# Kernel optimization log

Hardware: AMD Instinct MI355X
Metric: run time of the kernel (lower is better)

The kernel has to match this reference:

```python
import jax, jax.numpy as jnp
import numpy as np

B, L = 64, 200
NQ = 1024          # n_question == output_dim
NPID = 4096
D = 256            # q_embed_dim
H = 512            # hidden_dim
Q = 1024           # output_dim
L2 = 1e-05


def setup_inputs() -> dict:
    key = jax.random.key(0)
    ks = jax.random.split(key, 20)
    q_data = jax.random.randint(ks[0], (B, L), 1, NQ + 1)          # question ids in [1, NQ]
    ans = jax.random.randint(ks[1], (B, L), 0, 2)
    qa_data = q_data + NQ * ans                                     # encoded (q, answer)
    pid_data = jax.random.randint(ks[2], (B, L), 0, NPID + 1)
    matrix = jax.random.uniform(ks[3], (Q, Q), jnp.float32) * 0.05  # p_c_relations
    u = jax.random.uniform(ks[4], (B, L))
    target = jnp.where(u < 0.1, -1.0, jnp.where(u < 0.55, 0.0, 1.0)).astype(jnp.float32)
    s = 0.05
    q_emb = jax.random.normal(ks[5], (NQ + 1, D), jnp.float32) * s
    qa_emb = jax.random.normal(ks[6], (2, D), jnp.float32) * s
    q_emb_diff = jax.random.normal(ks[7], (NQ + 1, D), jnp.float32) * s
    qa_emb_diff = jax.random.normal(ks[8], (2 * NQ + 1, D), jnp.float32) * s
    diff_parm = jax.random.normal(ks[9], (NPID + 1, 1), jnp.float32) * s
    gs = 1.0 / np.sqrt(H).astype(np.float32)
    w_ih = jax.random.uniform(ks[10], (3 * H, 2 * D), jnp.float32, -gs, gs)
    w_hh = jax.random.uniform(ks[11], (3 * H, H), jnp.float32, -gs, gs)
    b_ih = jax.random.uniform(ks[12], (3 * H,), jnp.float32, -gs, gs)
    b_hh = jax.random.uniform(ks[13], (3 * H,), jnp.float32, -gs, gs)
    fc_w = jax.random.normal(ks[14], (Q, H), jnp.float32) * 0.02
    fc_b = jnp.zeros((Q,), jnp.float32)
    return dict(q_data=q_data, qa_data=qa_data, pid_data=pid_data, matrix=matrix,
                target=target, q_emb=q_emb, qa_emb=qa_emb, q_emb_diff=q_emb_diff,
                qa_emb_diff=qa_emb_diff, diff_parm=diff_parm, w_ih=w_ih, w_hh=w_hh,
                b_ih=b_ih, b_hh=b_hh, fc_w=fc_w, fc_b=fc_b)


def _gru(x, w_ih, w_hh, b_ih, b_hh):
    # PyTorch GRU, single layer, batch_first. x: [B, L, In]
    xg = jnp.einsum('bli,gi->blg', x, w_ih) + b_ih          # [B, L, 3H]
    def step(h, xg_t):
        hg = h @ w_hh.T + b_hh
        xr, xz, xn = jnp.split(xg_t, 3, axis=-1)
        hr, hz, hn = jnp.split(hg, 3, axis=-1)
        r = jax.nn.sigmoid(xr + hr)
        z = jax.nn.sigmoid(xz + hz)
        n = jnp.tanh(xn + r * hn)
        h_new = (1.0 - z) * n + z * h
        return h_new, h_new
    h0 = jnp.zeros((x.shape[0], w_hh.shape[1]), x.dtype)
    _, hs = jax.lax.scan(step, h0, xg.transpose(1, 0, 2))
    return hs.transpose(1, 0, 2)                             # [B, L, H]


def reference(q_data, qa_data, pid_data, matrix, target, q_emb, qa_emb,
              q_emb_diff, qa_emb_diff, diff_parm, w_ih, w_hh, b_ih, b_hh,
              fc_w, fc_b):
    q_embed = q_emb[q_data]                                  # [B, L, D]
    qa = (qa_data - q_data) // NQ                            # answer in {0,1}
    qa_embed = qa_emb[qa] + q_embed
    pid_embed = diff_parm[pid_data]                          # [B, L, 1]
    q_embed2 = q_embed + pid_embed * q_emb_diff[q_data]
    qa_embed2 = qa_embed + pid_embed * qa_emb_diff[qa]
    c_reg = (pid_embed ** 2).sum() * L2

    x = jnp.concatenate([qa_embed2, q_embed2], axis=-1)      # [B, L, 2D]
    gru_out = _gru(x, w_ih, w_hh, b_ih, b_hh)
    gru_out = jnp.einsum('blh,qh->blq', gru_out, fc_w) + fc_b  # [B, L, Q]

    got = jnp.einsum('blq,kq->blk', gru_out, matrix)         # [B, L, Q]
    master = jnp.where(got >= 0.4, 1.0, got)                 # threshold-to-1 only
    # mastery of the question asked at step t: master[b, t, q-1]
    mvals = jnp.take_along_axis(master, (q_data - 1)[..., None], axis=2)[..., 0]  # [B, L]

    f32 = jnp.float32
    eq = (q_data[:, :, None] == q_data[:, None, :]).astype(f32)   # [B, t, k]
    t_idx = jnp.arange(L)
    tri_strict = (t_idx[:, None] > t_idx[None, :]).astype(f32)    # k < t
    tri_incl = (t_idx[:, None] >= t_idx[None, :]).astype(f32)     # k <= t
    mast = (mvals == 1.0).astype(f32)
    notm = (mvals == 0.0).astype(f32)
    qa1 = (qa == 1).astype(f32)
    qa0 = 1.0 - qa1
    base = eq * tri_strict                                        # [B, L, L]
    mc = jnp.einsum('btk,bk->bt', base, qa1 * mast)   # master_correct
    mi = jnp.einsum('btk,bk->bt', base, qa0 * mast)   # master_incorrect
    nmc = jnp.einsum('btk,bk->bt', base, qa0 * notm)  # no_master_correct
    aa = jnp.einsum('btk,tk->bt', eq, tri_incl)       # answered_all (>= 1)

    arB = jnp.arange(B)
    idx = q_data - 1

    def dina_step(carry, xs):
        guess, slip = carry                            # [B, Q] each
        i_t, m_t, qa_t, mc_t, mi_t, nmc_t, aa_t = xs   # [B] each
        g_upd = jnp.where(m_t == 1.0, mc_t / aa_t,
                          jnp.where(qa_t == 0, 1.0 - nmc_t / aa_t, nmc_t / aa_t))
        upd_slip = (m_t == 1.0) & (qa_t == 0)
        new_g = jnp.where(upd_slip, guess[arB, i_t], g_upd)
        new_s = jnp.where(upd_slip, mi_t / aa_t, slip[arB, i_t])
        guess = guess.at[arB, i_t].set(new_g)
        slip = slip.at[arB, i_t].set(new_s)
        p = (1.0 - new_s) * (m_t * new_g + (1.0 - new_s) * (1.0 - m_t))
        return (guess, slip), p

    init = (jnp.zeros((B, Q), f32), jnp.zeros((B, Q), f32))
    xs = (idx.T, mvals.T, qa.T, mc.T, mi.T, nmc.T, aa.T)
    _, ps = jax.lax.scan(dina_step, init, xs)          # [L, B]
    preds = ps.T.reshape(-1)                           # [B*L]

    labels = target.reshape(-1)
    mask = labels > -0.9
    preds_d = jax.lax.stop_gradient(preds)             # torch detaches via torch.tensor()
    mse_sum = (((preds_d - labels) ** 2) * mask.astype(f32)).sum()
    loss = mse_sum + c_reg
    return (loss, jax.nn.sigmoid(preds_d), mask.sum())
```

## Files before the change

### kernel.cpp

```cpp
#include <hip/hip_runtime.h>
#include <hip/hip_bf16.h>
#include <math.h>

#define BB 64
#define LL 200
#define NQ 1024
#define DD 256
#define HH 512
#define QQ 1024
#define G3 1536
#define BL 12800
#define GBLK 256

#define OFF_ACC   ((size_t)0)
#define OFF_CELLS ((size_t)16)
#define OFF_HA    ((size_t)1056)
#define OFF_AQ    (OFF_HA + 65536)
#define OFF_DQ    (OFF_AQ + 1574400)
#define OFF_BQA   (OFF_DQ + 1574400)
#define OFF_CQA   (OFF_BQA + 3072)
#define OFF_WSUM  (OFF_CQA + 3072)
#define OFF_FCWT  (OFF_WSUM + 393216)
#define OFF_M2    (OFF_FCWT + 524288)
#define OFF_MB    (OFF_M2 + 524288)
#define OFF_XG    (OFF_MB + 1024)
#define OFF_GRUT  (OFF_XG + 19660800)
#define OFF_QINT  (OFF_GRUT + 6553600)
#define OFF_QAINT (OFF_QINT + 12800)
#define OFF_PIDF  (OFF_QAINT + 12800)
#define OFF_MVAL  (OFF_PIDF + 12800)
#define OFF_MC    (OFF_MVAL + 12800)
#define OFF_MI    (OFF_MC + 12800)
#define OFF_NMC   (OFF_MI + 12800)
#define OFF_AA    (OFF_NMC + 12800)
#define OFF_PREDS (OFF_AA + 12800)

typedef float f32x4 __attribute__((ext_vector_type(4)));

__device__ __forceinline__ float wave_sum64(float v) {
    #pragma unroll
    for (int o = 32; o > 0; o >>= 1) v += __shfl_down(v, o, 64);
    return v;
}

__device__ __forceinline__ f32x4 llc_load4(const float* p) {
    f32x4 v;
    asm volatile("global_load_dwordx4 %0, %1, off sc0 sc1" : "=v"(v) : "v"(p));
    return v;
}
__device__ __forceinline__ void llc_wait2(f32x4& a, f32x4& b) {
    asm volatile("s_waitcnt vmcnt(0)" : "+v"(a), "+v"(b));
}
__device__ __forceinline__ void llc_store1(float* p, float v) {
    asm volatile("global_store_dword %0, %1, off sc0 sc1" :: "v"(p), "v"(v) : "memory");
}

__device__ __forceinline__ float quad_sum(float v) {
    float t1 = __int_as_float(__builtin_amdgcn_update_dpp(
        0, __float_as_int(v), 0xB1, 0xF, 0xF, true));
    v += t1;
    float t2 = __int_as_float(__builtin_amdgcn_update_dpp(
        0, __float_as_int(v), 0x4E, 0xF, 0xF, true));
    return v + t2;
}

__global__ __launch_bounds__(256) void wsum_kernel(const float* __restrict__ w_ih,
                                                   float* __restrict__ wsum)
{
    int g = blockIdx.x, d = threadIdx.x;
    wsum[(size_t)g * DD + d] = w_ih[(size_t)g * 2 * DD + d] + w_ih[(size_t)g * 2 * DD + DD + d];
}

__device__ __forceinline__ void gemm_nt_body(
    const float* __restrict__ A, int lda, const float* __restrict__ B, int ldb,
    float* __restrict__ C, int ldc, int M, int N, int K,
    const float* __restrict__ bias, int bm, int bn, int tid,
    float (*As)[129], float (*Bs)[65])
{
    const int tx = tid & 15, ty = tid >> 4;
    const int mm = tid >> 4, kk = tid & 15;
    float acc[8][4] = {};
    float ar[8], br[4];
    #pragma unroll
    for (int i = 0; i < 8; ++i) {
        int m = bm + mm + 16 * i;
        ar[i] = (m < M) ? A[(size_t)m * lda + kk] : 0.f;
    }
    #pragma unroll
    for (int i = 0; i < 4; ++i) {
        int n = bn + mm + 16 * i;
        br[i] = (n < N) ? B[(size_t)n * ldb + kk] : 0.f;
    }
    for (int k0 = 0; k0 < K; k0 += 16) {
        #pragma unroll
        for (int i = 0; i < 8; ++i) As[kk][mm + 16 * i] = ar[i];
        #pragma unroll
        for (int i = 0; i < 4; ++i) Bs[kk][mm + 16 * i] = br[i];
        __syncthreads();
        int kn = k0 + 16;
        if (kn < K) {
            #pragma unroll
            for (int i = 0; i < 8; ++i) {
                int m = bm + mm + 16 * i;
                ar[i] = (m < M) ? A[(size_t)m * lda + kn + kk] : 0.f;
            }
            #pragma unroll
            for (int i = 0; i < 4; ++i) {
                int n = bn + mm + 16 * i;
                br[i] = (n < N) ? B[(size_t)n * ldb + kn + kk] : 0.f;
            }
        }
        #pragma unroll
        for (int kq = 0; kq < 16; ++kq) {
            float a[8], b[4];
            #pragma unroll
            for (int i = 0; i < 8; ++i) a[i] = As[kq][ty * 8 + i];
            #pragma unroll
            for (int j = 0; j < 4; ++j) b[j] = Bs[kq][tx * 4 + j];
            #pragma unroll
            for (int i = 0; i < 8; ++i)
                #pragma unroll
                for (int j = 0; j < 4; ++j) acc[i][j] += a[i] * b[j];
        }
        __syncthreads();
    }
    #pragma unroll
    for (int i = 0; i < 8; ++i) {
        int m = bm + ty * 8 + i;
        if (m >= M) continue;
        #pragma unroll
        for (int j = 0; j < 4; ++j) {
            int n = bn + tx * 4 + j;
            if (n >= N) continue;
            C[(size_t)m * ldc + n] = acc[i][j] + (bias ? bias[n] : 0.f);
        }
    }
}

__global__ __launch_bounds__(256) void prep_all(
    const float* __restrict__ q_emb, const float* __restrict__ q_emb_diff,
    const float* __restrict__ qa_emb, const float* __restrict__ qa_emb_diff,
    const float* __restrict__ wsum, const float* __restrict__ w_ih,
    const float* __restrict__ b_ih,
    float* __restrict__ Aq, float* __restrict__ Dq,
    float* __restrict__ Bqa, float* __restrict__ Cqa,
    const float* __restrict__ matrix, const float* __restrict__ fc_w,
    const float* __restrict__ fc_b, float* __restrict__ M2, float* __restrict__ mb,
    const int* __restrict__ q_data, const int* __restrict__ qa_data,
    const int* __restrict__ pid_data, const float* __restrict__ diff_parm,
    int* __restrict__ qint, int* __restrict__ qaint, float* __restrict__ pidf,
    float* __restrict__ acc_g)
{
    __shared__ float As[16][129];
    __shared__ float Bs[16][65];
    __shared__ float sm[4];
    const int tid = threadIdx.x;
    const int widx = blockIdx.x;

    if (widx < 432) {
        const int z = widx >= 216;
        const int w2 = z ? widx - 216 : widx;
        const int bm = (w2 / 24) * 128, bn = (w2 % 24) * 64;
        gemm_nt_body(z ? q_emb_diff : q_emb, DD,
                     z ? (w_ih + DD) : wsum, z ? 2 * DD : DD,
                     z ? Dq : Aq, G3, NQ + 1, G3, DD,
                     nullptr, bm, bn, tid, As, Bs);
        return;
    }
    if (widx < 480) {
        const int w2 = widx - 432;
        const int z = w2 >= 24;
        const int bn = (z ? w2 - 24 : w2) * 64;
        gemm_nt_body(z ? qa_emb_diff : qa_emb, DD,
                     w_ih, 2 * DD,
                     z ? Cqa : Bqa, G3, 2, G3, DD,
                     z ? nullptr : b_ih, 0, bn, tid, As, Bs);
        return;
    }
    if (widx < 608) {
        const int w2 = widx - 480;
        const int bm = (w2 >> 3) * 64, bn = (w2 & 7) * 64;
        const int kk = tid & 15, mm = tid >> 4;
        const int nb = tid & 63, kb2 = tid >> 6;
        const int tx = tid & 15, ty = tid >> 4;
        float acc[4][4] = {};
        for (int k0 = 0; k0 < QQ; k0 += 16) {
            if (k0) __syncthreads();
            #pragma unroll
            for (int i = 0; i < 4; ++i)
                As[kk][mm + 16 * i] = matrix[(size_t)(bm + mm + 16 * i) * QQ + k0 + kk];
            #pragma unroll
            for (int i = 0; i < 4; ++i)
                Bs[kb2 + 4 * i][nb] = fc_w[(size_t)(k0 + kb2 + 4 * i) * HH + bn + nb];
            __syncthreads();
            #pragma unroll
            for (int kq = 0; kq < 16; ++kq) {
                float a[4], b[4];
                #pragma unroll
                for (int i = 0; i < 4; ++i) a[i] = As[kq][ty * 4 + i];
                #pragma unroll
                for (int j = 0; j < 4; ++j) b[j] = Bs[kq][tx * 4 + j];
                #pragma unroll
                for (int i = 0; i < 4; ++i)
                    #pragma unroll
                    for (int j = 0; j < 4; ++j) acc[i][j] += a[i] * b[j];
            }
        }
        #pragma unroll
        for (int i = 0; i < 4; ++i)
            #pragma unroll
            for (int j = 0; j < 4; ++j)
                M2[(size_t)(bm + ty * 4 + i) * HH + bn + tx * 4 + j] = acc[i][j];
        return;
    }
    if (widx < 612) {
        const int wv2 = tid >> 6, lane2 = tid & 63;
        const int kb = (widx - 608) * 256 + wv2 * 64;
        for (int i = 0; i < 64; ++i) {
            const float* mrow = matrix + (size_t)(kb + i) * QQ;
            float sacc = 0.f;
            #pragma unroll
            for (int j = 0; j < 16; ++j)
                sacc += mrow[lane2 + 64 * j] * fc_b[lane2 + 64 * j];
            sacc = wave_sum64(sacc);
            if (lane2 == 0) mb[kb + i] = sacc;
        }
        return;
    }
    {
        int r = (widx - 612) * 256 + tid;
        float pp = 0.f;
        if (r < BL) {
            int q = q_data[r];
            qint[r] = q;
            qaint[r] = (qa_data[r] - q) / NQ;
            float pid = diff_parm[pid_data[r]];
            pidf[r] = pid;
            pp = pid * pid;
        }
        pp = wave_sum64(pp);
        int lane = tid & 63, w = tid >> 6;
        if (lane == 0) sm[w] = pp;
        __syncthreads();
        if (tid == 0) atomicAdd(&acc_g[0], sm[0] + sm[1] + sm[2] + sm[3]);
    }
}

__global__ __launch_bounds__(512) void gru_persist(
    const float* __restrict__ Aq,
    const float* __restrict__ Dq,
    const float* __restrict__ Bqa,
    const float* __restrict__ Cqa,
    const int* __restrict__ qint,
    const int* __restrict__ qaint,
    const float* __restrict__ pidf,
    const float* __restrict__ w_hh,
    const float* __restrict__ b_hh,
    float* __restrict__ hA,
    const float* __restrict__ M2,
    const float* __restrict__ mbv,
    float* __restrict__ mval,
    unsigned int* __restrict__ cells)
{
    __shared__ float hs[8][512];
    __shared__ float part[8][3][16][8];
    __shared__ float bqs[2][3][16];
    __shared__ float cqs[2][3][16];
    __shared__ int smq[8][200];
    __shared__ int smqa[8][200];
    __shared__ float smp[8][200];

    const int tid = threadIdx.x;
    const int bid = blockIdx.x;
    const int bg = bid >> 5;
    const int ug = bid & 31;
    const int j0 = ug * 16;
    const int wv = tid >> 6;
    const int lane = tid & 63;
    const int g = lane >> 2;
    const int s = lane & 3;

    if (tid < 96) {
        const int qa = tid / 48, rem = tid - qa * 48;
        const int gate = rem >> 4, u = rem & 15;
        bqs[qa][gate][u] = Bqa[(size_t)qa * G3 + gate * HH + j0 + u];
        cqs[qa][gate][u] = Cqa[(size_t)qa * G3 + gate * HH + j0 + u];
    }
    for (int i = tid; i < 8 * LL; i += 512) {
        const int c = i / LL, tt = i - c * LL;
        const int col = bg * 8 + c;
        smq[c][tt] = qint[col * LL + tt];
        smqa[c][tt] = qaint[col * LL + tt];
        smp[c][tt] = pidf[col * LL + tt];
    }

    f32x4 ws4[3][4];
    #pragma unroll
    for (int gate = 0; gate < 3; ++gate)
        #pragma unroll
        for (int q = 0; q < 4; ++q)
            ws4[gate][q] = *(const f32x4*)&w_hh[
                (size_t)(gate * HH + j0 + g) * HH + wv * 64 + q * 16 + s * 4];

    const int eu = tid >> 3;
    const int eb = tid & 7;
    float bhr = 0.f, bhz = 0.f, bhn = 0.f;
    if (tid < 128) {
        bhr = b_hh[j0 + eu];
        bhz = b_hh[HH + j0 + eu];
        bhn = b_hh[2 * HH + j0 + eu];
    }

    const int b0 = lane >> 4;
    const int c0 = (lane & 15) * 4;

    __syncthreads();

    for (int t = 0; t < LL; ++t) {
        float xr = 0.f, xz = 0.f, xn = 0.f;
        if (tid < 128) {
            const int q = smq[eb][t];
            const int qa = smqa[eb][t];
            const float pid = smp[eb][t];
            const float* aq = Aq + (size_t)q * G3 + j0 + eu;
            const float* dq = Dq + (size_t)q * G3 + j0 + eu;
            float ar_ = aq[0], az_ = aq[HH], an_ = aq[2 * HH];
            float dr_ = dq[0], dz_ = dq[HH], dn_ = dq[2 * HH];
            xr = ar_ + bqs[qa][0][eu] + pid * (cqs[qa][0][eu] + dr_);
            xz = az_ + bqs[qa][1][eu] + pid * (cqs[qa][1][eu] + dz_);
            xn = an_ + bqs[qa][2][eu] + pid * (cqs[qa][2][eu] + dn_);
        }
        if (t && tid < 64) {
            const unsigned want = (unsigned)t;
            for (;;) {
                unsigned v = want;
                if (lane < 32)
                    v = __hip_atomic_load(&cells[(bg * 32 + lane) * 4],
                                          __ATOMIC_RELAXED, __HIP_MEMORY_SCOPE_AGENT);
                if (__all((int)(v >= want))) break;
                __builtin_amdgcn_s_sleep(2);
            }
        }
        __syncthreads();

        {
            const float* hcur = hA + (size_t)(t & 1) * (HH * BB);
            const float* p0 = hcur + (size_t)(bg * 8 + b0) * HH + wv * 64 + c0;
            f32x4 va = llc_load4(p0);
            f32x4 vb = llc_load4(p0 + 4 * HH);
            llc_wait2(va, vb);
            *(f32x4*)&hs[wv][b0 * 64 + ((c0 + 8 * b0) & 63)] = va;
            *(f32x4*)&hs[wv][(b0 + 4) * 64 + ((c0 + 8 * b0 + 32) & 63)] = vb;
        }

        float acc[3][8];
        #pragma unroll
        for (int gate = 0; gate < 3; ++gate) {
            #pragma unroll
            for (int b = 0; b < 8; ++b) acc[gate][b] = 0.f;
        }
        #pragma unroll
        for (int q = 0; q < 4; ++q) {
            const int cb = q * 16 + s * 4;
            #pragma unroll
            for (int b = 0; b < 8; ++b) {
                f32x4 h4 = *(const f32x4*)&hs[wv][b * 64 + ((cb + 8 * b) & 63)];
                #pragma unroll
                for (int gate = 0; gate < 3; ++gate) {
                    acc[gate][b] += ws4[gate][q].x * h4.x + ws4[gate][q].y * h4.y
                                  + ws4[gate][q].z * h4.z + ws4[gate][q].w * h4.w;
                }
            }
        }

        #pragma unroll
        for (int gate = 0; gate < 3; ++gate)
            #pragma unroll
            for (int b = 0; b < 8; ++b)
                acc[gate][b] = quad_sum(acc[gate][b]);

        if (s < 3) {
            const int rot = (2 * ((g >> 2) + s)) & 7;
            #pragma unroll
            for (int hp = 0; hp < 4; ++hp) {
                const int b = hp * 2;
                float e0 = (s == 0) ? acc[0][b]     : (s == 1) ? acc[1][b]     : acc[2][b];
                float e1 = (s == 0) ? acc[0][b + 1] : (s == 1) ? acc[1][b + 1] : acc[2][b + 1];
                const int bp = (b + rot) & 7;
                *(float2*)&part[wv][s][g][bp] = make_float2(e0, e1);
            }
        }
        __syncthreads();

        if (wv == 2 && ug < 8 && t >= 1) {
            const int mvb = ug;
            const int q = smq[mvb][t - 1] - 1;
            const float* m2r = M2 + (size_t)q * HH + lane * 8;
            f32x4 ma = *(const f32x4*)m2r;
            f32x4 mc4 = *(const f32x4*)(m2r + 4);
            float sacc = 0.f;
            #pragma unroll
            for (int j = 0; j < 8; ++j) {
                const int k = lane * 8 + j;
                const float hv = hs[k >> 6][mvb * 64 + (((k & 63) + 8 * mvb) & 63)];
                const float mvw = (j == 0) ? ma.x : (j == 1) ? ma.y : (j == 2) ? ma.z
                                : (j == 3) ? ma.w : (j == 4) ? mc4.x : (j == 5) ? mc4.y
                                : (j == 6) ? mc4.z : mc4.w;
                sacc += hv * mvw;
            }
            sacc = wave_sum64(sacc);
            if (lane == 0) {
                float sv = sacc + mbv[q];
                mval[(bg * 8 + mvb) * LL + (t - 1)] = (sv >= 0.4f) ? 1.0f : sv;
            }
        }

        if (tid < 128) {
            const int rb = eu >> 2;
            const int bp0 = (eb + 2 * (rb + 0)) & 7;
            const int bp1 = (eb + 2 * (rb + 1)) & 7;
            const int bp2 = (eb + 2 * (rb + 2)) & 7;
            float sg0 = 0.f, sg1 = 0.f, sg2 = 0.f;
            #pragma unroll
            for (int w = 0; w < 8; ++w) {
                sg0 += part[w][0][eu][bp0];
                sg1 += part[w][1][eu][bp1];
                sg2 += part[w][2][eu][bp2];
            }
            const int ku = j0 + eu;
            float hprev = hs[ku >> 6][eb * 64 + (((ku & 63) + 8 * eb) & 63)];
            float rg = 1.f / (1.f + expf(-(xr + sg0 + bhr)));
            float zg = 1.f / (1.f + expf(-(xz + sg1 + bhz)));
            float ng = tanhf(xn + rg * (sg2 + bhn));
            float hn = (1.f - zg) * ng + zg * hprev;
            llc_store1(hA + (size_t)((t + 1) & 1) * (HH * BB)
                          + (size_t)(bg * 8 + eb) * HH + ku, hn);
            asm volatile("s_waitcnt vmcnt(0)" ::: "memory");
        }
        __syncthreads();
        if (tid == 0)
            __hip_atomic_store(&cells[bid * 4], (unsigned)(t + 1),
                               __ATOMIC_RELAXED, __HIP_MEMORY_SCOPE_AGENT);
    }

    if (ug < 8) {
        if (tid < 64) {
            const unsigned want = (unsigned)LL;
            for (;;) {
                unsigned v = want;
                if (lane < 32)
                    v = __hip_atomic_load(&cells[(bg * 32 + lane) * 4],
                                          __ATOMIC_RELAXED, __HIP_MEMORY_SCOPE_AGENT);
                if (__all((int)(v >= want))) break;
                __builtin_amdgcn_s_sleep(2);
            }
        }
        __syncthreads();
        {
            const float* hcur = hA + (size_t)(LL & 1) * (HH * BB);
            const float* p0 = hcur + (size_t)(bg * 8 + b0) * HH + wv * 64 + c0;
            f32x4 va = llc_load4(p0);
            f32x4 vb = llc_load4(p0 + 4 * HH);
            llc_wait2(va, vb);
            *(f32x4*)&hs[wv][b0 * 64 + ((c0 + 8 * b0) & 63)] = va;
            *(f32x4*)&hs[wv][(b0 + 4) * 64 + ((c0 + 8 * b0 + 32) & 63)] = vb;
        }
        __syncthreads();
        if (wv == 2) {
            const int mvb = ug;
            const int q = smq[mvb][LL - 1] - 1;
            const float* m2r = M2 + (size_t)q * HH + lane * 8;
            f32x4 ma = *(const f32x4*)m2r;
            f32x4 mc4 = *(const f32x4*)(m2r + 4);
            float sacc = 0.f;
            #pragma unroll
            for (int j = 0; j < 8; ++j) {
                const int k = lane * 8 + j;
                const float hv = hs[k >> 6][mvb * 64 + (((k & 63) + 8 * mvb) & 63)];
                const float mvw = (j == 0) ? ma.x : (j == 1) ? ma.y : (j == 2) ? ma.z
                                : (j == 3) ? ma.w : (j == 4) ? mc4.x : (j == 5) ? mc4.y
                                : (j == 6) ? mc4.z : mc4.w;
                sacc += hv * mvw;
            }
            sacc = wave_sum64(sacc);
            if (lane == 0) {
                float sv = sacc + mbv[q];
                mval[(bg * 8 + mvb) * LL + (LL - 1)] = (sv >= 0.4f) ? 1.0f : sv;
            }
        }
    }
}

__global__ __launch_bounds__(256) void statsdina_kernel(
    const int* __restrict__ qint, const int* __restrict__ qaint,
    const float* __restrict__ mval, float* __restrict__ preds)
{
    int b = blockIdx.x, tid = threadIdx.x;
    __shared__ float guess[QQ], slip[QQ];
    __shared__ int qs[LL];
    __shared__ int qas[LL];
    __shared__ float mv[LL], s_mc[LL], s_mi[LL], s_nmc[LL], s_aa[LL];
    for (int i = tid; i < QQ; i += 256) { guess[i] = 0.f; slip[i] = 0.f; }
    if (tid < LL) {
        qs[tid] = qint[b * LL + tid];
        qas[tid] = qaint[b * LL + tid];
        mv[tid] = mval[b * LL + tid];
    }
    __syncthreads();
    if (tid < LL) {
        int qt = qs[tid];
        float smc = 0.f, smi = 0.f, snmc = 0.f, saa = 0.f;
        for (int k = 0; k <= tid; ++k) {
            if (qs[k] == qt) {
                saa += 1.f;
                if (k < tid) {
                    float mk = (mv[k] == 1.f) ? 1.f : 0.f;
                    float nk = (mv[k] == 0.f) ? 1.f : 0.f;
                    float a1 = (qas[k] == 1) ? 1.f : 0.f;
                    smc += a1 * mk;
                    smi += (1.f - a1) * mk;
                    snmc += (1.f - a1) * nk;
                }
            }
        }
        s_mc[tid] = smc;
        s_mi[tid] = smi;
        s_nmc[tid] = snmc;
        s_aa[tid] = saa;
    }
    __syncthreads();
    if (tid == 0) {
        for (int t = 0; t < LL; ++t) {
            int i = qs[t] - 1;
            float m = mv[t];
            int qa = qas[t];
            float aat = s_aa[t];
            float g_upd = (m == 1.f) ? s_mc[t] / aat
                          : ((qa == 0) ? 1.f - s_nmc[t] / aat : s_nmc[t] / aat);
            bool us = (m == 1.f) && (qa == 0);
            float ng = us ? guess[i] : g_upd;
            float ns = us ? s_mi[t] / aat : slip[i];
            guess[i] = ng;
            slip[i] = ns;
            preds[b * LL + t] = (1.f - ns) * (m * ng + (1.f - ns) * (1.f - m));
        }
    }
}

__global__ __launch_bounds__(256) void loss_kernel(
    const float* __restrict__ preds, const float* __restrict__ target,
    float* __restrict__ out, float* __restrict__ acc)
{
    int r = blockIdx.x * 256 + threadIdx.x;
    float lm = 0.f, lc = 0.f;
    if (r < BL) {
        float p = preds[r], lab = target[r];
        float msk = (lab > -0.9f) ? 1.f : 0.f;
        float d = p - lab;
        lm = d * d * msk;
        lc = msk;
        out[1 + r] = 1.f / (1.f + expf(-p));
    }
    lm = wave_sum64(lm);
    lc = wave_sum64(lc);
    __shared__ float sm[4], sc[4];
    int lane = threadIdx.x & 63, w = threadIdx.x >> 6;
    if (lane == 0) { sm[w] = lm; sc[w] = lc; }
    __syncthreads();
    if (threadIdx.x == 0) {
        atomicAdd(&acc[1], sm[0] + sm[1] + sm[2] + sm[3]);
        atomicAdd(&acc[2], sc[0] + sc[1] + sc[2] + sc[3]);
    }
}

__global__ void final_kernel(const float* __restrict__ acc, float* __restrict__ out)
{
    out[0] = acc[1] + acc[0] * 1e-5f;
    out[1 + BL] = acc[2];
}

extern "C" void kernel_launch(void* const* d_in, const int* in_sizes, int n_in,
                              void* d_out, int out_size, void* d_ws, size_t ws_size,
                              hipStream_t stream) {
    const int* q_data = (const int*)d_in[0];
    const int* qa_data = (const int*)d_in[1];
    const int* pid_data = (const int*)d_in[2];
    const float* matrix = (const float*)d_in[3];
    const float* target = (const float*)d_in[4];
    const float* q_emb = (const float*)d_in[5];
    const float* qa_emb = (const float*)d_in[6];
    const float* q_emb_diff = (const float*)d_in[7];
    const float* qa_emb_diff = (const float*)d_in[8];
    const float* diff_parm = (const float*)d_in[9];
    const float* w_ih = (const float*)d_in[10];
    const float* w_hh = (const float*)d_in[11];
    const float* b_ih = (const float*)d_in[12];
    const float* b_hh = (const float*)d_in[13];
    const float* fc_w = (const float*)d_in[14];
    const float* fc_b = (const float*)d_in[15];
    float* out = (float*)d_out;
    float* W = (float*)d_ws;

    float* acc = W + OFF_ACC;
    unsigned int* cells = (unsigned int*)(W + OFF_CELLS);
    float* hA = W + OFF_HA;
    float* Aq = W + OFF_AQ;
    float* Dq = W + OFF_DQ;
    float* Bqa = W + OFF_BQA;
    float* Cqa = W + OFF_CQA;
    float* wsum = W + OFF_WSUM;
    float* M2 = W + OFF_M2;
    float* mb = W + OFF_MB;
    int* qint = (int*)(W + OFF_QINT);
    int* qaint = (int*)(W + OFF_QAINT);
    float* pidf = W + OFF_PIDF;
    float* mval = W + OFF_MVAL;
    float* preds = W + OFF_PREDS;

    hipMemsetAsync(W, 0, (OFF_HA + 2 * HH * BB) * sizeof(float), stream);

    wsum_kernel<<<G3, 256, 0, stream>>>(w_ih, wsum);

    prep_all<<<662, 256, 0, stream>>>(
        q_emb, q_emb_diff, qa_emb, qa_emb_diff, wsum, w_ih, b_ih,
        Aq, Dq, Bqa, Cqa, matrix, fc_w, fc_b, M2, mb,
        q_data, qa_data, pid_data, diff_parm, qint, qaint, pidf, acc);

    gru_persist<<<GBLK, 512, 0, stream>>>(Aq, Dq, Bqa, Cqa, qint, qaint, pidf,
                                          w_hh, b_hh, hA, M2, mb, mval, cells);

    statsdina_kernel<<<BB, 256, 0, stream>>>(qint, qaint, mval, preds);
    loss_kernel<<<50, 256, 0, stream>>>(preds, target, out, acc);
    final_kernel<<<1, 1, 0, stream>>>(acc, out);
}
```

Baseline: 1.079 ms.

## Fuse DINA stats, loss and finalization into persistent GRU kernel; drop launches

Moves the DINA scan, loss reduction and final output write into the tail of the persistent GRU kernel, using shared memory for mastery values instead of a global buffer. It also folds the w_ih half-sum into the GEMM B-load, replaces part of the memset with zeroing blocks in prep_all, reorders prep_all so the M2 GEMM blocks come first, and prefetches M2 rows before the per-step barrier spin. This removes four kernel launches and some global round trips, at the cost of serial DINA work running on only 64 of the persistent blocks and a last-block atomic counter to finalize.

```diff
diff --git a/kernel.cpp b/kernel.cpp
--- a/kernel.cpp
+++ b/kernel.cpp
@@ -23,17 +23,9 @@
 #define OFF_FCWT  (OFF_WSUM + 393216)
 #define OFF_M2    (OFF_FCWT + 524288)
 #define OFF_MB    (OFF_M2 + 524288)
-#define OFF_XG    (OFF_MB + 1024)
-#define OFF_GRUT  (OFF_XG + 19660800)
-#define OFF_QINT  (OFF_GRUT + 6553600)
+#define OFF_QINT  (OFF_MB + 1024)
 #define OFF_QAINT (OFF_QINT + 12800)
 #define OFF_PIDF  (OFF_QAINT + 12800)
-#define OFF_MVAL  (OFF_PIDF + 12800)
-#define OFF_MC    (OFF_MVAL + 12800)
-#define OFF_MI    (OFF_MC + 12800)
-#define OFF_NMC   (OFF_MI + 12800)
-#define OFF_AA    (OFF_NMC + 12800)
-#define OFF_PREDS (OFF_AA + 12800)
 
 typedef float f32x4 __attribute__((ext_vector_type(4)));
 
@@ -64,17 +56,10 @@
     return v + t2;
 }
 
-__global__ __launch_bounds__(256) void wsum_kernel(const float* __restrict__ w_ih,
-                                                   float* __restrict__ wsum)
-{
-    int g = blockIdx.x, d = threadIdx.x;
-    wsum[(size_t)g * DD + d] = w_ih[(size_t)g * 2 * DD + d] + w_ih[(size_t)g * 2 * DD + DD + d];
-}
-
 __device__ __forceinline__ void gemm_nt_body(
     const float* __restrict__ A, int lda, const float* __restrict__ B, int ldb,
     float* __restrict__ C, int ldc, int M, int N, int K,
-    const float* __restrict__ bias, int bm, int bn, int tid,
+    const float* __restrict__ bias, int bm, int bn, int tid, bool sumB,
     float (*As)[129], float (*Bs)[65])
 {
     const int tx = tid & 15, ty = tid >> 4;
@@ -89,7 +74,8 @@
     #pragma unroll
     for (int i = 0; i < 4; ++i) {
         int n = bn + mm + 16 * i;
-        br[i] = (n < N) ? B[(size_t)n * ldb + kk] : 0.f;
+        br[i] = (n < N) ? (sumB ? (B[(size_t)n * ldb + kk] + B[(size_t)n * ldb + DD + kk])
+                                : B[(size_t)n * ldb + kk]) : 0.f;
     }
     for (int k0 = 0; k0 < K; k0 += 16) {
         #pragma unroll
@@ -107,7 +93,9 @@
             #pragma unroll
             for (int i = 0; i < 4; ++i) {
                 int n = bn + mm + 16 * i;
-                br[i] = (n < N) ? B[(size_t)n * ldb + kn + kk] : 0.f;
+                br[i] = (n < N) ? (sumB ? (B[(size_t)n * ldb + kn + kk]
+                                           + B[(size_t)n * ldb + DD + kn + kk])
+                                        : B[(size_t)n * ldb + kn + kk]) : 0.f;
             }
         }
         #pragma unroll
@@ -140,8 +128,7 @@
 __global__ __launch_bounds__(256) void prep_all(
     const float* __restrict__ q_emb, const float* __restrict__ q_emb_diff,
     const float* __restrict__ qa_emb, const float* __restrict__ qa_emb_diff,
-    const float* __restrict__ wsum, const float* __restrict__ w_ih,
-    const float* __restrict__ b_ih,
+    const float* __restrict__ w_ih, const float* __restrict__ b_ih,
     float* __restrict__ Aq, float* __restrict__ Dq,
     float* __restrict__ Bqa, float* __restrict__ Cqa,
     const float* __restrict__ matrix, const float* __restrict__ fc_w,
@@ -149,7 +136,7 @@
     const int* __restrict__ q_data, const int* __restrict__ qa_data,
     const int* __restrict__ pid_data, const float* __restrict__ diff_parm,
     int* __restrict__ qint, int* __restrict__ qaint, float* __restrict__ pidf,
-    float* __restrict__ acc_g)
+    float* __restrict__ acc_g, float* __restrict__ hA)
 {
     __shared__ float As[16][129];
     __shared__ float Bs[16][65];
@@ -157,29 +144,8 @@
     const int tid = threadIdx.x;
     const int widx = blockIdx.x;
 
-    if (widx < 432) {
-        const int z = widx >= 216;
-        const int w2 = z ? widx - 216 : widx;
-        const int bm = (w2 / 24) * 128, bn = (w2 % 24) * 64;
-        gemm_nt_body(z ? q_emb_diff : q_emb, DD,
-                     z ? (w_ih + DD) : wsum, z ? 2 * DD : DD,
-                     z ? Dq : Aq, G3, NQ + 1, G3, DD,
-                     nullptr, bm, bn, tid, As, Bs);
-        return;
-    }
-    if (widx < 480) {
-        const int w2 = widx - 432;
-        const int z = w2 >= 24;
-        const int bn = (z ? w2 - 24 : w2) * 64;
-        gemm_nt_body(z ? qa_emb_diff : qa_emb, DD,
-                     w_ih, 2 * DD,
-                     z ? Cqa : Bqa, G3, 2, G3, DD,
-                     z ? nullptr : b_ih, 0, bn, tid, As, Bs);
-        return;
-    }
-    if (widx < 608) {
-        const int w2 = widx - 480;
-        const int bm = (w2 >> 3) * 64, bn = (w2 & 7) * 64;
+    if (widx < 128) {
+        const int bm = (widx >> 3) * 64, bn = (widx & 7) * 64;
         const int kk = tid & 15, mm = tid >> 4;
         const int nb = tid & 63, kb2 = tid >> 6;
         const int tx = tid & 15, ty = tid >> 4;
@@ -213,6 +179,27 @@
                 M2[(size_t)(bm + ty * 4 + i) * HH + bn + tx * 4 + j] = acc[i][j];
         return;
     }
+    if (widx < 560) {
+        const int w2 = widx - 128;
+        const int z = w2 >= 216;
+        const int w3 = z ? w2 - 216 : w2;
+        const int bm = (w3 / 24) * 128, bn = (w3 % 24) * 64;
+        gemm_nt_body(z ? q_emb_diff : q_emb, DD,
+                     z ? (w_ih + DD) : w_ih, 2 * DD,
+                     z ? Dq : Aq, G3, NQ + 1, G3, DD,
+                     nullptr, bm, bn, tid, !z, As, Bs);
+        return;
+    }
+    if (widx < 608) {
+        const int w2 = widx - 560;
+        const int z = w2 >= 24;
+        const int bn = (z ? w2 - 24 : w2) * 64;
+        gemm_nt_body(z ? qa_emb_diff : qa_emb, DD,
+                     w_ih, 2 * DD,
+                     z ? Cqa : Bqa, G3, 2, G3, DD,
+                     z ? nullptr : b_ih, 0, bn, tid, false, As, Bs);
+        return;
+    }
     if (widx < 612) {
         const int wv2 = tid >> 6, lane2 = tid & 63;
         const int kb = (widx - 608) * 256 + wv2 * 64;
@@ -227,7 +214,7 @@
         }
         return;
     }
-    {
+    if (widx < 662) {
         int r = (widx - 612) * 256 + tid;
         float pp = 0.f;
         if (r < BL) {
@@ -243,6 +230,12 @@
         if (lane == 0) sm[w] = pp;
         __syncthreads();
         if (tid == 0) atomicAdd(&acc_g[0], sm[0] + sm[1] + sm[2] + sm[3]);
+        return;
+    }
+    {
+        float* dst = hA + (size_t)(widx - 662) * 4096 + tid;
+        #pragma unroll
+        for (int i = 0; i < 16; ++i) dst[i * 256] = 0.f;
     }
 }
 
@@ -259,8 +252,10 @@
     float* __restrict__ hA,
     const float* __restrict__ M2,
     const float* __restrict__ mbv,
-    float* __restrict__ mval,
-    unsigned int* __restrict__ cells)
+    unsigned int* __restrict__ cells,
+    const float* __restrict__ target,
+    float* __restrict__ out,
+    float* __restrict__ acc_g)
 {
     __shared__ float hs[8][512];
     __shared__ float part[8][3][16][8];
@@ -269,6 +264,7 @@
     __shared__ int smq[8][200];
     __shared__ int smqa[8][200];
     __shared__ float smp[8][200];
+    __shared__ float mvbuf[LL];
 
     const int tid = threadIdx.x;
     const int bid = blockIdx.x;
@@ -330,6 +326,15 @@
             xz = az_ + bqs[qa][1][eu] + pid * (cqs[qa][1][eu] + dz_);
             xn = an_ + bqs[qa][2][eu] + pid * (cqs[qa][2][eu] + dn_);
         }
+        f32x4 m2a = {0.f, 0.f, 0.f, 0.f}, m2b = {0.f, 0.f, 0.f, 0.f};
+        float mbq = 0.f;
+        if (wv == 2 && ug < 8 && t >= 1) {
+            const int q = smq[ug][t - 1] - 1;
+            const float* m2r = M2 + (size_t)q * HH + lane * 8;
+            m2a = *(const f32x4*)m2r;
+            m2b = *(const f32x4*)(m2r + 4);
+            mbq = mbv[q];
+        }
         if (t && tid < 64) {
             const unsigned want = (unsigned)t;
             for (;;) {
@@ -393,25 +398,20 @@
         __syncthreads();
 
         if (wv == 2 && ug < 8 && t >= 1) {
-            const int mvb = ug;
-            const int q = smq[mvb][t - 1] - 1;
-            const float* m2r = M2 + (size_t)q * HH + lane * 8;
-            f32x4 ma = *(const f32x4*)m2r;
-            f32x4 mc4 = *(const f32x4*)(m2r + 4);
             float sacc = 0.f;
             #pragma unroll
             for (int j = 0; j < 8; ++j) {
                 const int k = lane * 8 + j;
-                const float hv = hs[k >> 6][mvb * 64 + (((k & 63) + 8 * mvb) & 63)];
-                const float mvw = (j == 0) ? ma.x : (j == 1) ? ma.y : (j == 2) ? ma.z
-                                : (j == 3) ? ma.w : (j == 4) ? mc4.x : (j == 5) ? mc4.y
-                                : (j == 6) ? mc4.z : mc4.w;
+                const float hv = hs[k >> 6][ug * 64 + (((k & 63) + 8 * ug) & 63)];
+                const float mvw = (j == 0) ? m2a.x : (j == 1) ? m2a.y : (j == 2) ? m2a.z
+                                : (j == 3) ? m2a.w : (j == 4) ? m2b.x : (j == 5) ? m2b.y
+                                : (j == 6) ? m2b.z : m2b.w;
                 sacc += hv * mvw;
             }
             sacc = wave_sum64(sacc);
             if (lane == 0) {
-                float sv = sacc + mbv[q];
-                mval[(bg * 8 + mvb) * LL + (t - 1)] = (sv >= 0.4f) ? 1.0f : sv;
+                float sv = sacc + mbq;
+                mvbuf[t - 1] = (sv >= 0.4f) ? 1.0f : sv;
             }
         }
 
@@ -443,80 +443,73 @@
                                __ATOMIC_RELAXED, __HIP_MEMORY_SCOPE_AGENT);
     }
 
-    if (ug < 8) {
-        if (tid < 64) {
-            const unsigned want = (unsigned)LL;
-            for (;;) {
-                unsigned v = want;
-                if (lane < 32)
-                    v = __hip_atomic_load(&cells[(bg * 32 + lane) * 4],
-                                          __ATOMIC_RELAXED, __HIP_MEMORY_SCOPE_AGENT);
-                if (__all((int)(v >= want))) break;
-                __builtin_amdgcn_s_sleep(2);
-            }
-        }
-        __syncthreads();
-        {
-            const float* hcur = hA + (size_t)(LL & 1) * (HH * BB);
-            const float* p0 = hcur + (size_t)(bg * 8 + b0) * HH + wv * 64 + c0;
-            f32x4 va = llc_load4(p0);
-            f32x4 vb = llc_load4(p0 + 4 * HH);
-            llc_wait2(va, vb);
-            *(f32x4*)&hs[wv][b0 * 64 + ((c0 + 8 * b0) & 63)] = va;
-            *(f32x4*)&hs[wv][(b0 + 4) * 64 + ((c0 + 8 * b0 + 32) & 63)] = vb;
-        }
-        __syncthreads();
-        if (wv == 2) {
-            const int mvb = ug;
-            const int q = smq[mvb][LL - 1] - 1;
-            const float* m2r = M2 + (size_t)q * HH + lane * 8;
-            f32x4 ma = *(const f32x4*)m2r;
-            f32x4 mc4 = *(const f32x4*)(m2r + 4);
-            float sacc = 0.f;
-            #pragma unroll
-            for (int j = 0; j < 8; ++j) {
-                const int k = lane * 8 + j;
-                const float hv = hs[k >> 6][mvb * 64 + (((k & 63) + 8 * mvb) & 63)];
-                const float mvw = (j == 0) ? ma.x : (j == 1) ? ma.y : (j == 2) ? ma.z
-                                : (j == 3) ? ma.w : (j == 4) ? mc4.x : (j == 5) ? mc4.y
-                                : (j == 6) ? mc4.z : mc4.w;
-                sacc += hv * mvw;
-            }
-            sacc = wave_sum64(sacc);
-            if (lane == 0) {
-                float sv = sacc + mbv[q];
-                mval[(bg * 8 + mvb) * LL + (LL - 1)] = (sv >= 0.4f) ? 1.0f : sv;
-            }
-        }
-    }
-}
-
-__global__ __launch_bounds__(256) void statsdina_kernel(
-    const int* __restrict__ qint, const int* __restrict__ qaint,
-    const float* __restrict__ mval, float* __restrict__ preds)
-{
-    int b = blockIdx.x, tid = threadIdx.x;
-    __shared__ float guess[QQ], slip[QQ];
-    __shared__ int qs[LL];
-    __shared__ int qas[LL];
-    __shared__ float mv[LL], s_mc[LL], s_mi[LL], s_nmc[LL], s_aa[LL];
-    for (int i = tid; i < QQ; i += 256) { guess[i] = 0.f; slip[i] = 0.f; }
+    if (ug >= 8) return;
+    if (tid < 64) {
+        const unsigned want = (unsigned)LL;
+        for (;;) {
+            unsigned v = want;
+            if (lane < 32)
+                v = __hip_atomic_load(&cells[(bg * 32 + lane) * 4],
+                                      __ATOMIC_RELAXED, __HIP_MEMORY_SCOPE_AGENT);
+            if (__all((int)(v >= want))) break;
+            __builtin_amdgcn_s_sleep(2);
+        }
+    }
+    __syncthreads();
+    {
+        const float* hcur = hA + (size_t)(LL & 1) * (HH * BB);
+        const float* p0 = hcur + (size_t)(bg * 8 + b0) * HH + wv * 64 + c0;
+        f32x4 va = llc_load4(p0);
+        f32x4 vb = llc_load4(p0 + 4 * HH);
+        llc_wait2(va, vb);
+        *(f32x4*)&hs[wv][b0 * 64 + ((c0 + 8 * b0) & 63)] = va;
+        *(f32x4*)&hs[wv][(b0 + 4) * 64 + ((c0 + 8 * b0 + 32) & 63)] = vb;
+    }
+    __syncthreads();
+    if (wv == 2) {
+        const int q = smq[ug][LL - 1] - 1;
+        const float* m2r = M2 + (size_t)q * HH + lane * 8;
+        f32x4 ma = *(const f32x4*)m2r;
+        f32x4 mc4 = *(const f32x4*)(m2r + 4);
+        float sacc = 0.f;
+        #pragma unroll
+        for (int j = 0; j < 8; ++j) {
+            const int k = lane * 8 + j;
+            const float hv = hs[k >> 6][ug * 64 + (((k & 63) + 8 * ug) & 63)];
+            const float mvw = (j == 0) ? ma.x : (j == 1) ? ma.y : (j == 2) ? ma.z
+                            : (j == 3) ? ma.w : (j == 4) ? mc4.x : (j == 5) ? mc4.y
+                            : (j == 6) ? mc4.z : mc4.w;
+            sacc += hv * mvw;
+        }
+        sacc = wave_sum64(sacc);
+        if (lane == 0) {
+            float sv = sacc + mbv[q];
+            mvbuf[LL - 1] = (sv >= 0.4f) ? 1.0f : sv;
+        }
+    }
+    __syncthreads();
+
+    const int bq = bg * 8 + ug;
+    float* guess = &hs[0][0];
+    float* slip = &hs[2][0];
+    float* preds_l = &hs[4][0];
+    float* s_mc = &part[0][0][0][0];
+    float* s_mi = s_mc + 256;
+    float* s_nmc = s_mc + 512;
+    float* s_aa = s_mc + 768;
+    float* sred = &bqs[0][0][0];
+    float* cred = sred + 8;
+    for (int i = tid; i < QQ; i += 512) { guess[i] = 0.f; slip[i] = 0.f; }
     if (tid < LL) {
-        qs[tid] = qint[b * LL + tid];
-        qas[tid] = qaint[b * LL + tid];
-        mv[tid] = mval[b * LL + tid];
-    }
-    __syncthreads();
-    if (tid < LL) {
-        int qt = qs[tid];
+        const int qt = smq[ug][tid];
         float smc = 0.f, smi = 0.f, snmc = 0.f, saa = 0.f;
         for (int k = 0; k <= tid; ++k) {
-            if (qs[k] == qt) {
+            if (smq[ug][k] == qt) {
                 saa += 1.f;
                 if (k < tid) {
-                    float mk = (mv[k] == 1.f) ? 1.f : 0.f;
-                    float nk = (mv[k] == 0.f) ? 1.f : 0.f;
-                    float a1 = (qas[k] == 1) ? 1.f : 0.f;
+                    float mk = (mvbuf[k] == 1.f) ? 1.f : 0.f;
+                    float nk = (mvbuf[k] == 0.f) ? 1.f : 0.f;
+                    float a1 = (smqa[ug][k] == 1) ? 1.f : 0.f;
                     smc += a1 * mk;
                     smi += (1.f - a1) * mk;
                     snmc += (1.f - a1) * nk;
@@ -531,10 +524,10 @@
     __syncthreads();
     if (tid == 0) {
         for (int t = 0; t < LL; ++t) {
-            int i = qs[t] - 1;
-            float m = mv[t];
-            int qa = qas[t];
-            float aat = s_aa[t];
+            const int i = smq[ug][t] - 1;
+            const float m = mvbuf[t];
+            const int qa = smqa[ug][t];
+            const float aat = s_aa[t];
             float g_upd = (m == 1.f) ? s_mc[t] / aat
                           : ((qa == 0) ? 1.f - s_nmc[t] / aat : s_nmc[t] / aat);
             bool us = (m == 1.f) && (qa == 0);
@@ -542,41 +535,40 @@
             float ns = us ? s_mi[t] / aat : slip[i];
             guess[i] = ng;
             slip[i] = ns;
-            preds[b * LL + t] = (1.f - ns) * (m * ng + (1.f - ns) * (1.f - m));
-        }
-    }
-}
-
-__global__ __launch_bounds__(256) void loss_kernel(
-    const float* __restrict__ preds, const float* __restrict__ target,
-    float* __restrict__ out, float* __restrict__ acc)
-{
-    int r = blockIdx.x * 256 + threadIdx.x;
-    float lm = 0.f, lc = 0.f;
-    if (r < BL) {
-        float p = preds[r], lab = target[r];
-        float msk = (lab > -0.9f) ? 1.f : 0.f;
-        float d = p - lab;
-        lm = d * d * msk;
-        lc = msk;
-        out[1 + r] = 1.f / (1.f + expf(-p));
-    }
-    lm = wave_sum64(lm);
-    lc = wave_sum64(lc);
-    __shared__ float sm[4], sc[4];
-    int lane = threadIdx.x & 63, w = threadIdx.x >> 6;
-    if (lane == 0) { sm[w] = lm; sc[w] = lc; }
+            preds_l[t] = (1.f - ns) * (m * ng + (1.f - ns) * (1.f - m));
+        }
+    }
     __syncthreads();
-    if (threadIdx.x == 0) {
-        atomicAdd(&acc[1], sm[0] + sm[1] + sm[2] + sm[3]);
-        atomicAdd(&acc[2], sc[0] + sc[1] + sc[2] + sc[3]);
-    }
-}
-
-__global__ void final_kernel(const float* __restrict__ acc, float* __restrict__ out)
-{
-    out[0] = acc[1] + acc[0] * 1e-5f;
-    out[1 + BL] = acc[2];
+    if (tid < 256) {
+        float lm = 0.f, lc = 0.f;
+        if (tid < LL) {
+            const float p = preds_l[tid];
+            const float lab = target[bq * LL + tid];
+            const float msk = (lab > -0.9f) ? 1.f : 0.f;
+            const float d = p - lab;
+            lm = d * d * msk;
+            lc = msk;
+            out[1 + bq * LL + tid] = 1.f / (1.f + expf(-p));
+        }
+        lm = wave_sum64(lm);
+        lc = wave_sum64(lc);
+        if (lane == 0) { sred[wv] = lm; cred[wv] = lc; }
+    }
+    __syncthreads();
+    if (tid == 0) {
+        atomicAdd(&acc_g[1], sred[0] + sred[1] + sred[2] + sred[3]);
+        atomicAdd(&acc_g[2], cred[0] + cred[1] + cred[2] + cred[3]);
+        const unsigned old = __hip_atomic_fetch_add(&cells[1021], 1u,
+                                                    __ATOMIC_ACQ_REL,
+                                                    __HIP_MEMORY_SCOPE_AGENT);
+        if (old == 63) {
+            float a0 = __hip_atomic_load(&acc_g[0], __ATOMIC_RELAXED, __HIP_MEMORY_SCOPE_AGENT);
+            float a1 = __hip_atomic_load(&acc_g[1], __ATOMIC_RELAXED, __HIP_MEMORY_SCOPE_AGENT);
+            float a2 = __hip_atomic_load(&acc_g[2], __ATOMIC_RELAXED, __HIP_MEMORY_SCOPE_AGENT);
+            out[0] = a1 + a0 * 1e-5f;
+            out[1 + BL] = a2;
+        }
+    }
 }
 
 extern "C" void kernel_launch(void* const* d_in, const int* in_sizes, int n_in,
@@ -608,28 +600,20 @@
     float* Dq = W + OFF_DQ;
     float* Bqa = W + OFF_BQA;
     float* Cqa = W + OFF_CQA;
-    float* wsum = W + OFF_WSUM;
     float* M2 = W + OFF_M2;
     float* mb = W + OFF_MB;
     int* qint = (int*)(W + OFF_QINT);
     int* qaint = (int*)(W + OFF_QAINT);
     float* pidf = W + OFF_PIDF;
-    float* mval = W + OFF_MVAL;
-    float* preds = W + OFF_PREDS;
-
-    hipMemsetAsync(W, 0, (OFF_HA + 2 * HH * BB) * sizeof(float), stream);
-
-    wsum_kernel<<<G3, 256, 0, stream>>>(w_ih, wsum);
-
-    prep_all<<<662, 256, 0, stream>>>(
-        q_emb, q_emb_diff, qa_emb, qa_emb_diff, wsum, w_ih, b_ih,
+
+    hipMemsetAsync(W, 0, 1056 * sizeof(float), stream);
+
+    prep_all<<<678, 256, 0, stream>>>(
+        q_emb, q_emb_diff, qa_emb, qa_emb_diff, w_ih, b_ih,
         Aq, Dq, Bqa, Cqa, matrix, fc_w, fc_b, M2, mb,
-        q_data, qa_data, pid_data, diff_parm, qint, qaint, pidf, acc);
+        q_data, qa_data, pid_data, diff_parm, qint, qaint, pidf, acc, hA);
 
     gru_persist<<<GBLK, 512, 0, stream>>>(Aq, Dq, Bqa, Cqa, qint, qaint, pidf,
-                                          w_hh, b_hh, hA, M2, mb, mval, cells);
-
-    statsdina_kernel<<<BB, 256, 0, stream>>>(qint, qaint, mval, preds);
-    loss_kernel<<<50, 256, 0, stream>>>(preds, target, out, acc);
-    final_kernel<<<1, 1, 0, stream>>>(acc, out);
-}
+                                          w_hh, b_hh, hA, M2, mb, cells,
+                                          target, out, acc);
+}
```

Result: faster. 1.005 ms (-6.9%).
